# Kernel optimization log

Hardware: AMD Instinct MI355X
Metric: run time of the kernel (lower is better)

## Reference

```python
import jax, jax.numpy as jnp
import numpy as np
from jax import lax

B, CIN, COUT, H, W, K, LAT = 16, 256, 256, 64, 64, 3, 512
EPS = 1e-8
LRELU_SLOPE = 0.2
ACT_GAIN = float(np.sqrt(2.0))


def setup_inputs() -> dict:
    key = jax.random.key(0)
    ks = jax.random.split(key, 6)
    # equalized-lr (implicit_lreq) init: weights already carry std = gain/sqrt(fan_in)
    conv_std = np.sqrt(2.0) / np.sqrt(CIN * K * K)   # gain=sqrt(2)
    style_std = 1.0 / np.sqrt(LAT)                    # style affine uses gain=1
    return {
        "x": jax.random.normal(ks[0], (B, CIN, H, W), jnp.float32),
        "style": jax.random.normal(ks[1], (B, LAT), jnp.float32),
        "noise": jax.random.normal(ks[2], (B, 1, H, W), jnp.float32),
        "weight": jax.random.normal(ks[3], (COUT, CIN, K, K), jnp.float32) * conv_std,
        "style_w": jax.random.normal(ks[4], (LAT, CIN), jnp.float32) * style_std,
        "style_b": jnp.ones((CIN,), jnp.float32),   # bias_initial = 1 (StyleGAN2)
        "bias": jnp.zeros((COUT,), jnp.float32),
        "noise_weight": jax.random.normal(ks[5], (1,), jnp.float32) * 0.1,
    }


def reference(x, style, noise, weight, style_w, style_b, bias, noise_weight):
    b, cin, h, w_ = x.shape
    cout = weight.shape[0]
    # style affine -> per-sample, per-input-channel modulation scales
    s = style @ style_w + style_b                              # [B, Cin]
    # modulate per-sample weights
    wmod = weight[None] * s[:, None, :, None, None]            # [B, Cout, Cin, K, K]
    # demodulate
    d = lax.rsqrt(jnp.sum(wmod * wmod, axis=(2, 3, 4)) + EPS)  # [B, Cout]
    wmod = wmod * d[:, :, None, None, None]
    # batch-as-groups conv2d
    xg = x.reshape(1, b * cin, h, w_)
    wg = wmod.reshape(b * cout, cin, K, K)
    out = lax.conv_general_dilated(
        xg, wg, window_strides=(1, 1), padding=[(1, 1), (1, 1)],
        feature_group_count=b,
        dimension_numbers=("NCHW", "OIHW", "NCHW"),
    ).reshape(b, cout, h, w_)
    # noise injection + bias + leaky relu with sqrt(2) gain
    out = out + noise * noise_weight[0] + bias[None, :, None, None]
    return jax.nn.leaky_relu(out, LRELU_SLOPE) * ACT_GAIN
```

## Files before the change

kernel.cpp:

```cpp
#include <hip/hip_runtime.h>
#include <hip/hip_bf16.h>

typedef __bf16 bf16x8 __attribute__((ext_vector_type(8)));
typedef float f32x4 __attribute__((ext_vector_type(4)));

#define LAT 512

__device__ __forceinline__ void async_load16(const void* g, void* l) {
  __builtin_amdgcn_global_load_lds(
      (const __attribute__((address_space(1))) unsigned int*)g,
      (__attribute__((address_space(3))) unsigned int*)l, 16, 0, 0);
}

__global__ void style_kernel(const float* __restrict__ style,
                             const float* __restrict__ style_w,
                             const float* __restrict__ style_b,
                             float* __restrict__ smod) {
  int b = blockIdx.x, cin = threadIdx.x;
  float acc = style_b[cin];
  const float* st = style + b * LAT;
  for (int l = 0; l < LAT; ++l)
    acc = fmaf(st[l], style_w[l * 256 + cin], acc);
  smod[b * 256 + cin] = acc;
}

__global__ void modw_kernel(const float* __restrict__ weight,
                            const float* __restrict__ smod,
                            __hip_bfloat16* __restrict__ wmod) {
  int cout = blockIdx.x, b = blockIdx.y;
  int cin = threadIdx.x;
  float s = smod[b * 256 + cin];
  const float* wp = weight + ((size_t)cout * 256 + cin) * 9;
  float w[9];
  float ss = 0.f;
#pragma unroll
  for (int j = 0; j < 9; ++j) { w[j] = wp[j]; ss = fmaf(w[j], w[j], ss); }
  ss *= s * s;
#pragma unroll
  for (int off = 32; off > 0; off >>= 1) ss += __shfl_down(ss, off, 64);
  __shared__ float red[4];
  __shared__ float dsh;
  int lane = threadIdx.x & 63, wv = threadIdx.x >> 6;
  if (lane == 0) red[wv] = ss;
  __syncthreads();
  if (threadIdx.x == 0) dsh = rsqrtf(red[0] + red[1] + red[2] + red[3] + 1e-8f);
  __syncthreads();
  float d = dsh * s;
  size_t obase = ((size_t)(b * 9) * 256 + cout) * 256 + cin;
#pragma unroll
  for (int j = 0; j < 9; ++j)
    wmod[obase + (size_t)j * 65536] = __float2bfloat16(w[j] * d);
}

__global__ void border_kernel(__hip_bfloat16* __restrict__ xt) {
  int bp = blockIdx.x;
  int b = blockIdx.y;
  int h, w;
  if (bp < 66)       { h = 0;        w = bp; }
  else if (bp < 132) { h = 65;       w = bp - 66; }
  else if (bp < 196) { h = bp - 131; w = 0; }
  else               { h = bp - 195; w = 65; }
  xt[((size_t)(b * 66 + h) * 66 + w) * 256 + threadIdx.x] = __float2bfloat16(0.f);
}

__global__ void transpose_kernel(const float* __restrict__ x,
                                 __hip_bfloat16* __restrict__ xt) {
  __shared__ __hip_bfloat16 tile[64][258];
  int h = blockIdx.x, b = blockIdx.y, t = threadIdx.x;
  int w4 = (t & 15) * 4;
  int csub = t >> 4;
  for (int c0 = 0; c0 < 256; c0 += 16) {
    int cin = c0 + csub;
    const float4 v = *(const float4*)(x + (((size_t)(b * 256 + cin) * 64 + h) << 6) + w4);
    tile[w4 + 0][cin] = __float2bfloat16(v.x);
    tile[w4 + 1][cin] = __float2bfloat16(v.y);
    tile[w4 + 2][cin] = __float2bfloat16(v.z);
    tile[w4 + 3][cin] = __float2bfloat16(v.w);
  }
  __syncthreads();
  int wsub = t >> 7;
  int cpair = t & 127;
  size_t obase = ((size_t)(b * 66 + h + 1) * 66 + 1) * 256;
  for (int w0 = 0; w0 < 64; w0 += 2) {
    int w = w0 + wsub;
    unsigned int v = *(const unsigned int*)&tile[w][cpair * 2];
    *(unsigned int*)((__hip_bfloat16*)xt + obase + (size_t)w * 256 + cpair * 2) = v;
  }
}

__global__ __launch_bounds__(256, 2)
void conv_kernel(const __hip_bfloat16* __restrict__ wmod,
                 const __hip_bfloat16* __restrict__ xt,
                 const float* __restrict__ noise,
                 const float* __restrict__ bias,
                 const float* __restrict__ nwt,
                 float* __restrict__ out) {
  __shared__ __align__(16) char lds[32768];
  const int t = threadIdx.x;
  const int bx = blockIdx.x;
  const int cout0 = blockIdx.y * 128;
  const int b = blockIdx.z;

  size_t a_off[4], b_off[4];
  const size_t wbase = (size_t)b * 9 * 65536;
#pragma unroll
  for (int i = 0; i < 4; ++i) {
    int e = i * 256 + t;
    int m = e >> 3, c8 = e & 7;
    int gk8 = c8 ^ (m & 7);
    a_off[i] = (size_t)(cout0 + m) * 256 + gk8 * 8;
    int hrow = m >> 6, wcol = m & 63;
    b_off[i] = ((size_t)(b * 66 + bx * 2 + hrow) * 66 + wcol) * 256 + gk8 * 8;
  }

  const int lane = t & 63;
  const int wv = t >> 6;
  const int mw = (wv >> 1) * 64, nwl = (wv & 1) * 64;
  const int col = lane & 15, quad = lane >> 4;

  int aro[4][2], bro[4][2];
#pragma unroll
  for (int i = 0; i < 4; ++i) {
    int m = mw + i * 16 + col;
    int n = nwl + i * 16 + col;
#pragma unroll
    for (int ks = 0; ks < 2; ++ks) {
      int k8 = ks * 4 + quad;
      aro[i][ks] = (m * 8 + (k8 ^ (m & 7))) * 16;
      bro[i][ks] = 16384 + (n * 8 + (k8 ^ (n & 7))) * 16;
    }
  }

  f32x4 acc[4][4];
#pragma unroll
  for (int i = 0; i < 4; ++i)
#pragma unroll
    for (int j = 0; j < 4; ++j)
      acc[i][j] = (f32x4){0.f, 0.f, 0.f, 0.f};

  for (int s = 0; s < 9; ++s) {
    const int kh = s / 3, kw = s % 3;
    const size_t abase = wbase + (size_t)s * 65536;
    const size_t bbase = (size_t)(kh * 66 + kw) * 256;
    for (int kc = 0; kc < 4; ++kc) {
      __syncthreads();
#pragma unroll
      for (int i = 0; i < 4; ++i) {
        async_load16(wmod + abase + a_off[i] + kc * 64, lds + (i * 256 + t) * 16);
        async_load16(xt + bbase + b_off[i] + kc * 64, lds + 16384 + (i * 256 + t) * 16);
      }
      __syncthreads();
#pragma unroll
      for (int ks = 0; ks < 2; ++ks) {
        bf16x8 af[4], bfr[4];
#pragma unroll
        for (int i = 0; i < 4; ++i) af[i] = *(const bf16x8*)(lds + aro[i][ks]);
#pragma unroll
        for (int j = 0; j < 4; ++j) bfr[j] = *(const bf16x8*)(lds + bro[j][ks]);
#pragma unroll
        for (int i = 0; i < 4; ++i)
#pragma unroll
          for (int j = 0; j < 4; ++j)
            acc[i][j] = __builtin_amdgcn_mfma_f32_16x16x32_bf16(af[i], bfr[j], acc[i][j], 0, 0, 0);
      }
    }
  }

  const float nw0 = nwt[0];
  const int p0 = bx * 128;
  float nz[4];
#pragma unroll
  for (int j = 0; j < 4; ++j)
    nz[j] = noise[(b << 12) + p0 + nwl + j * 16 + col] * nw0;
#pragma unroll
  for (int i = 0; i < 4; ++i) {
    int mloc = mw + i * 16 + quad * 4;
#pragma unroll
    for (int j = 0; j < 4; ++j) {
      int p = p0 + nwl + j * 16 + col;
      f32x4 v = acc[i][j];
#pragma unroll
      for (int r = 0; r < 4; ++r) {
        int coutg = cout0 + mloc + r;
        float val = v[r] + nz[j] + bias[coutg];
        val = (val > 0.f ? val : 0.2f * val) * 1.4142135623730951f;
        out[(((size_t)(b * 256 + coutg)) << 12) + p] = val;
      }
    }
  }
}

extern "C" void kernel_launch(void* const* d_in, const int* in_sizes, int n_in,
                              void* d_out, int out_size, void* d_ws, size_t ws_size,
                              hipStream_t stream) {
  const float* x        = (const float*)d_in[0];
  const float* style    = (const float*)d_in[1];
  const float* noise    = (const float*)d_in[2];
  const float* weight   = (const float*)d_in[3];
  const float* style_w  = (const float*)d_in[4];
  const float* style_b  = (const float*)d_in[5];
  const float* bias     = (const float*)d_in[6];
  const float* noise_w  = (const float*)d_in[7];
  float* out = (float*)d_out;

  char* ws = (char*)d_ws;
  float* smod = (float*)ws;
  __hip_bfloat16* wmod = (__hip_bfloat16*)(ws + 16384);
  __hip_bfloat16* xt = (__hip_bfloat16*)(ws + 16384 + 18874368);

  style_kernel<<<16, 256, 0, stream>>>(style, style_w, style_b, smod);
  modw_kernel<<<dim3(256, 16), 256, 0, stream>>>(weight, smod, wmod);
  border_kernel<<<dim3(260, 16), 256, 0, stream>>>(xt);
  transpose_kernel<<<dim3(64, 16), 256, 0, stream>>>(x, xt);
  conv_kernel<<<dim3(32, 2, 16), 256, 0, stream>>>(wmod, xt, noise, bias, noise_w, out);
}
```

Baseline: 249.3 us.

## Double-buffer conv LDS tiles with async prefetch and remap block order

The conv kernel's LDS grows to two 32KB buffers, and the next K-stage is prefetched with global_load_lds while the current stage is computed. Manual vmcnt waits and raw s_barrier calls replace the two __syncthreads per stage, and s_setprio raises priority around the MFMA block. The block index is also remapped so neighbouring blocks spread differently, meant to improve L2 reuse of weights and inputs. The larger LDS footprint may cut occupancy below two blocks per CU, and the hand-written waitcnt logic adds a correctness risk.

Result: faster. 222.3 us (-10.8%).

```diff
diff --git a/kernel.cpp b/kernel.cpp
--- a/kernel.cpp
+++ b/kernel.cpp
@@ -95,11 +95,14 @@
                  const float* __restrict__ bias,
                  const float* __restrict__ nwt,
                  float* __restrict__ out) {
-  __shared__ __align__(16) char lds[32768];
+  __shared__ __align__(16) char lds[65536];
   const int t = threadIdx.x;
-  const int bx = blockIdx.x;
-  const int cout0 = blockIdx.y * 128;
-  const int b = blockIdx.z;
+
+  const int bid = blockIdx.x + (blockIdx.y << 5) + (blockIdx.z << 6);
+  const int nid = ((bid & 7) << 7) + (bid >> 3);
+  const int bx = nid & 31;
+  const int cout0 = ((nid >> 5) & 1) << 7;
+  const int b = nid >> 6;
 
   size_t a_off[4], b_off[4];
   const size_t wbase = (size_t)b * 9 * 65536;
@@ -138,32 +141,53 @@
     for (int j = 0; j < 4; ++j)
       acc[i][j] = (f32x4){0.f, 0.f, 0.f, 0.f};
 
-  for (int s = 0; s < 9; ++s) {
-    const int kh = s / 3, kw = s % 3;
-    const size_t abase = wbase + (size_t)s * 65536;
-    const size_t bbase = (size_t)(kh * 66 + kw) * 256;
-    for (int kc = 0; kc < 4; ++kc) {
-      __syncthreads();
-#pragma unroll
-      for (int i = 0; i < 4; ++i) {
-        async_load16(wmod + abase + a_off[i] + kc * 64, lds + (i * 256 + t) * 16);
-        async_load16(xt + bbase + b_off[i] + kc * 64, lds + 16384 + (i * 256 + t) * 16);
-      }
-      __syncthreads();
-#pragma unroll
-      for (int ks = 0; ks < 2; ++ks) {
-        bf16x8 af[4], bfr[4];
-#pragma unroll
-        for (int i = 0; i < 4; ++i) af[i] = *(const bf16x8*)(lds + aro[i][ks]);
-#pragma unroll
-        for (int j = 0; j < 4; ++j) bfr[j] = *(const bf16x8*)(lds + bro[j][ks]);
-#pragma unroll
-        for (int i = 0; i < 4; ++i)
-#pragma unroll
-          for (int j = 0; j < 4; ++j)
-            acc[i][j] = __builtin_amdgcn_mfma_f32_16x16x32_bf16(af[i], bfr[j], acc[i][j], 0, 0, 0);
-      }
-    }
+  auto stage_fn = [&](int st, int bo) {
+    const int s9 = st >> 2, kc = st & 3;
+    const int kh = s9 / 3, kw = s9 - 3 * kh;
+    const size_t abase = wbase + ((size_t)s9 << 16) + (kc << 6);
+    const size_t bbase = (size_t)((kh * 66 + kw) << 8) + (kc << 6);
+#pragma unroll
+    for (int i = 0; i < 4; ++i) {
+      async_load16(wmod + abase + a_off[i], lds + bo + i * 4096 + t * 16);
+      async_load16(xt + bbase + b_off[i], lds + bo + 16384 + i * 4096 + t * 16);
+    }
+  };
+
+  auto compute_fn = [&](int bo) {
+#pragma unroll
+    for (int ks = 0; ks < 2; ++ks) {
+      bf16x8 af[4], bfr[4];
+#pragma unroll
+      for (int i = 0; i < 4; ++i) af[i] = *(const bf16x8*)(lds + bo + aro[i][ks]);
+#pragma unroll
+      for (int j = 0; j < 4; ++j) bfr[j] = *(const bf16x8*)(lds + bo + bro[j][ks]);
+#pragma unroll
+      for (int i = 0; i < 4; ++i)
+#pragma unroll
+        for (int j = 0; j < 4; ++j)
+          acc[i][j] = __builtin_amdgcn_mfma_f32_16x16x32_bf16(af[i], bfr[j], acc[i][j], 0, 0, 0);
+    }
+  };
+
+  stage_fn(0, 0);
+  stage_fn(1, 32768);
+
+#pragma unroll 2
+  for (int st = 0; st < 36; ++st) {
+    const int bo = (st & 1) << 15;
+    if (st == 35) {
+      asm volatile("s_waitcnt vmcnt(0)" ::: "memory");
+    } else {
+      asm volatile("s_waitcnt vmcnt(8)" ::: "memory");
+    }
+    __builtin_amdgcn_s_barrier();
+    __builtin_amdgcn_sched_barrier(0);
+    __builtin_amdgcn_s_setprio(1);
+    compute_fn(bo);
+    __builtin_amdgcn_s_setprio(0);
+    __builtin_amdgcn_s_barrier();
+    __builtin_amdgcn_sched_barrier(0);
+    if (st < 34) stage_fn(st + 2, bo);
   }
 
   const float nw0 = nwt[0];
```

## Double-buffer conv mainloop with larger N tile, reordered K loop and block swizzle

Applied to the files above, without the earlier changes.

The implicit-GEMM conv kernel now uses a 128x256 output tile per block, with each wave covering 64x128, and steps K in 32-wide chunks across all nine taps. Global-to-LDS async loads are issued two stages ahead into double buffers, synchronised with explicit vmcnt waits and raw barriers, and MFMA priority is raised during compute. Block IDs are remapped so neighbouring blocks share data for better L2 reuse, and bias is loaded as a float4. The aim is to hide load latency and raise arithmetic intensity, at the cost of more accumulator registers and LDS, which may lower occupancy, and halving the grid to 512 blocks.

New measurement: 226.7 us. 1.1x faster.

```diff
diff --git a/kernel.cpp b/kernel.cpp
--- a/kernel.cpp
+++ b/kernel.cpp
@@ -95,94 +95,133 @@
                  const float* __restrict__ bias,
                  const float* __restrict__ nwt,
                  float* __restrict__ out) {
-  __shared__ __align__(16) char lds[32768];
+  __shared__ __align__(16) char lds[49152];
   const int t = threadIdx.x;
-  const int bx = blockIdx.x;
-  const int cout0 = blockIdx.y * 128;
-  const int b = blockIdx.z;
-
-  size_t a_off[4], b_off[4];
-  const size_t wbase = (size_t)b * 9 * 65536;
-#pragma unroll
-  for (int i = 0; i < 4; ++i) {
-    int e = i * 256 + t;
-    int m = e >> 3, c8 = e & 7;
-    int gk8 = c8 ^ (m & 7);
-    a_off[i] = (size_t)(cout0 + m) * 256 + gk8 * 8;
-    int hrow = m >> 6, wcol = m & 63;
-    b_off[i] = ((size_t)(b * 66 + bx * 2 + hrow) * 66 + wcol) * 256 + gk8 * 8;
-  }
+
+  const int bid = blockIdx.x + (blockIdx.y << 4) + (blockIdx.z << 5);
+  const int nid = ((bid & 7) << 6) + (bid >> 3);
+  const int sp = nid & 15;
+  const int cout0 = ((nid >> 4) & 1) << 7;
+  const int b = nid >> 5;
 
   const int lane = t & 63;
   const int wv = t >> 6;
-  const int mw = (wv >> 1) * 64, nwl = (wv & 1) * 64;
+  const int mw = (wv >> 1) << 6;
+  const int nwl = (wv & 1) << 7;
   const int col = lane & 15, quad = lane >> 4;
 
-  int aro[4][2], bro[4][2];
+  unsigned asrc[2];
+#pragma unroll
+  for (int it = 0; it < 2; ++it) {
+    int ch = it * 256 + t;
+    int m = ch >> 2, qs = ch & 3;
+    int k8 = qs ^ ((m >> 1) & 3);
+    asrc[it] = (unsigned)((cout0 + m) * 256 + k8 * 8);
+  }
+  const size_t wbase = (size_t)b * 9 * 65536;
+
+  unsigned bsrc0[4];
+#pragma unroll
+  for (int it = 0; it < 4; ++it) {
+    int ch = it * 256 + t;
+    int n = ch >> 2, qs = ch & 3;
+    int k8 = qs ^ ((n >> 1) & 3);
+    bsrc0[it] = (unsigned)((((b * 66 + (sp << 2) + (n >> 6)) * 66 + (n & 63)) << 8) + k8 * 8);
+  }
+
+  int aro[4];
 #pragma unroll
   for (int i = 0; i < 4; ++i) {
     int m = mw + i * 16 + col;
-    int n = nwl + i * 16 + col;
-#pragma unroll
-    for (int ks = 0; ks < 2; ++ks) {
-      int k8 = ks * 4 + quad;
-      aro[i][ks] = (m * 8 + (k8 ^ (m & 7))) * 16;
-      bro[i][ks] = 16384 + (n * 8 + (k8 ^ (n & 7))) * 16;
-    }
-  }
-
-  f32x4 acc[4][4];
+    aro[i] = (m << 6) + ((quad ^ ((m >> 1) & 3)) << 4);
+  }
+  int bro[8];
+#pragma unroll
+  for (int j = 0; j < 8; ++j) {
+    int n = nwl + j * 16 + col;
+    bro[j] = (n << 6) + ((quad ^ ((n >> 1) & 3)) << 4);
+  }
+
+  f32x4 acc[4][8];
 #pragma unroll
   for (int i = 0; i < 4; ++i)
 #pragma unroll
-    for (int j = 0; j < 4; ++j)
+    for (int j = 0; j < 8; ++j)
       acc[i][j] = (f32x4){0.f, 0.f, 0.f, 0.f};
 
-  for (int s = 0; s < 9; ++s) {
-    const int kh = s / 3, kw = s % 3;
-    const size_t abase = wbase + (size_t)s * 65536;
-    const size_t bbase = (size_t)(kh * 66 + kw) * 256;
-    for (int kc = 0; kc < 4; ++kc) {
-      __syncthreads();
-#pragma unroll
-      for (int i = 0; i < 4; ++i) {
-        async_load16(wmod + abase + a_off[i] + kc * 64, lds + (i * 256 + t) * 16);
-        async_load16(xt + bbase + b_off[i] + kc * 64, lds + 16384 + (i * 256 + t) * 16);
-      }
-      __syncthreads();
-#pragma unroll
-      for (int ks = 0; ks < 2; ++ks) {
-        bf16x8 af[4], bfr[4];
-#pragma unroll
-        for (int i = 0; i < 4; ++i) af[i] = *(const bf16x8*)(lds + aro[i][ks]);
-#pragma unroll
-        for (int j = 0; j < 4; ++j) bfr[j] = *(const bf16x8*)(lds + bro[j][ks]);
-#pragma unroll
-        for (int i = 0; i < 4; ++i)
-#pragma unroll
-          for (int j = 0; j < 4; ++j)
-            acc[i][j] = __builtin_amdgcn_mfma_f32_16x16x32_bf16(af[i], bfr[j], acc[i][j], 0, 0, 0);
+  auto stage = [&](int kc, int tap, int buf) {
+    const int dtap = (tap / 3) * 66 + (tap % 3);
+    const __hip_bfloat16* asrcp = wmod + wbase + tap * 65536 + kc * 32;
+    const __hip_bfloat16* bsrcp = xt + (dtap << 8) + kc * 32;
+    char* adst = lds + buf * 8192 + t * 16;
+    char* bdst = lds + 16384 + buf * 16384 + t * 16;
+    async_load16(asrcp + asrc[0], adst);
+    async_load16(asrcp + asrc[1], adst + 4096);
+#pragma unroll
+    for (int it = 0; it < 4; ++it)
+      async_load16(bsrcp + bsrc0[it], bdst + it * 4096);
+  };
+
+  auto compute = [&](int buf) {
+    const char* A = lds + buf * 8192;
+    const char* Bb = lds + 16384 + buf * 16384;
+    bf16x8 af[4], bfr[8];
+#pragma unroll
+    for (int i = 0; i < 4; ++i) af[i] = *(const bf16x8*)(A + aro[i]);
+#pragma unroll
+    for (int j = 0; j < 8; ++j) bfr[j] = *(const bf16x8*)(Bb + bro[j]);
+#pragma unroll
+    for (int i = 0; i < 4; ++i)
+#pragma unroll
+      for (int j = 0; j < 8; ++j)
+        acc[i][j] = __builtin_amdgcn_mfma_f32_16x16x32_bf16(af[i], bfr[j], acc[i][j], 0, 0, 0);
+  };
+
+  stage(0, 0, 0);
+  __builtin_amdgcn_sched_barrier(0);
+  stage(0, 1, 1);
+  __builtin_amdgcn_sched_barrier(0);
+
+#pragma unroll
+  for (int kc = 0; kc < 8; ++kc) {
+#pragma unroll
+    for (int tap = 0; tap < 9; ++tap) {
+      const int s = kc * 9 + tap;
+      if (s == 71) asm volatile("s_waitcnt vmcnt(0)" ::: "memory");
+      else         asm volatile("s_waitcnt vmcnt(6)" ::: "memory");
+      __builtin_amdgcn_s_barrier();
+      __builtin_amdgcn_sched_barrier(0);
+      __builtin_amdgcn_s_setprio(1);
+      compute(s & 1);
+      __builtin_amdgcn_s_setprio(0);
+      __builtin_amdgcn_s_barrier();
+      __builtin_amdgcn_sched_barrier(0);
+      if (s <= 69) {
+        const int s2 = s + 2;
+        stage(s2 / 9, s2 % 9, s & 1);
+        __builtin_amdgcn_sched_barrier(0);
       }
     }
   }
 
   const float nw0 = nwt[0];
-  const int p0 = bx * 128;
-  float nz[4];
-#pragma unroll
-  for (int j = 0; j < 4; ++j)
-    nz[j] = noise[(b << 12) + p0 + nwl + j * 16 + col] * nw0;
+  float nz[8];
+#pragma unroll
+  for (int j = 0; j < 8; ++j)
+    nz[j] = noise[(b << 12) + (sp << 8) + nwl + j * 16 + col] * nw0;
 #pragma unroll
   for (int i = 0; i < 4; ++i) {
-    int mloc = mw + i * 16 + quad * 4;
-#pragma unroll
-    for (int j = 0; j < 4; ++j) {
-      int p = p0 + nwl + j * 16 + col;
+    const int mloc = mw + i * 16 + quad * 4;
+    const float4 b4 = *(const float4*)(bias + cout0 + mloc);
+#pragma unroll
+    for (int j = 0; j < 8; ++j) {
+      const int p = (sp << 8) + nwl + j * 16 + col;
       f32x4 v = acc[i][j];
+      const float bb[4] = {b4.x, b4.y, b4.z, b4.w};
 #pragma unroll
       for (int r = 0; r < 4; ++r) {
-        int coutg = cout0 + mloc + r;
-        float val = v[r] + nz[j] + bias[coutg];
+        const int coutg = cout0 + mloc + r;
+        float val = v[r] + nz[j] + bb[r];
         val = (val > 0.f ? val : 0.2f * val) * 1.4142135623730951f;
         out[(((size_t)(b * 256 + coutg)) << 12) + p] = val;
       }
@@ -212,5 +251,5 @@
   modw_kernel<<<dim3(256, 16), 256, 0, stream>>>(weight, smod, wmod);
   border_kernel<<<dim3(260, 16), 256, 0, stream>>>(xt);
   transpose_kernel<<<dim3(64, 16), 256, 0, stream>>>(x, xt);
-  conv_kernel<<<dim3(32, 2, 16), 256, 0, stream>>>(wmod, xt, noise, bias, noise_w, out);
-}
+  conv_kernel<<<dim3(16, 2, 16), 256, 0, stream>>>(wmod, xt, noise, bias, noise_w, out);
+}
```
